# Performance work log

Hardware: AMD Instinct MI355X
Metric: run time of the kernel (lower is better)

## Reference

```python
import jax, jax.numpy as jnp
import numpy as np
import math

D_MODEL = 1024
HEADS = 16
HEAD_DIM = D_MODEL // HEADS
BATCH = 2
SEQ = 2048


def setup_inputs() -> dict:
    key = jax.random.key(0)
    ks = jax.random.split(key, 6)
    scale = 1.0 / math.sqrt(D_MODEL)
    return {
        "x": jax.random.normal(ks[0], (BATCH, SEQ, D_MODEL), dtype=jnp.float32),
        "mask": jnp.zeros((SEQ, SEQ), dtype=jnp.float32),
        "w_qkv": jax.random.normal(ks[1], (D_MODEL, 3 * D_MODEL), dtype=jnp.float32) * scale,
        "b_qkv": jax.random.normal(ks[2], (3 * D_MODEL,), dtype=jnp.float32) * 0.01,
        "w_out": jax.random.normal(ks[3], (D_MODEL, D_MODEL), dtype=jnp.float32) * scale,
        "b_out": jax.random.normal(ks[4], (D_MODEL,), dtype=jnp.float32) * 0.01,
    }


def reference(x, mask, w_qkv, b_qkv, w_out, b_out):
    B, S, D = x.shape
    H, hd = HEADS, HEAD_DIM
    # fused QKV projection: [B,S,3D]
    qkv = x @ w_qkv + b_qkv
    # [B,S,H,3*hd] -> [B,H,S,3*hd]
    qkv = qkv.reshape(B, S, H, 3 * hd).transpose(0, 2, 1, 3)
    q, k, v = jnp.split(qkv, 3, axis=-1)  # each [B,H,S,hd]
    inv_sqrt_d = jnp.asarray(1.0 / math.sqrt(hd), dtype=x.dtype)
    scores = jnp.einsum("bhqd,bhkd->bhqk", q, k) * inv_sqrt_d
    # additive mask; [S,S] broadcasts identically in [H,B,S,S] or [B,H,S,S] layout
    scores = scores + mask
    attn = jax.nn.softmax(scores, axis=-1)
    vals = jnp.einsum("bhqk,bhkd->bhqd", attn, v)  # [B,H,S,hd]
    vals = vals.transpose(0, 2, 1, 3).reshape(B, S, H * hd)
    return vals @ w_out + b_out
```

## Files before the change

kernel.cpp:

```cpp
#include <hip/hip_runtime.h>


typedef __bf16 bf16;
typedef __bf16 bf16x2 __attribute__((ext_vector_type(2)));
typedef __bf16 bf16x4 __attribute__((ext_vector_type(4)));
typedef __bf16 bf16x8 __attribute__((ext_vector_type(8)));
typedef float f32x4 __attribute__((ext_vector_type(4)));
typedef float f32x16 __attribute__((ext_vector_type(16)));

#define MFMA(a, b, c) __builtin_amdgcn_mfma_f32_16x16x32_bf16((a), (b), (c), 0, 0, 0)
#define MFMA32(a, b, c) __builtin_amdgcn_mfma_f32_32x32x16_bf16((a), (b), (c), 0, 0, 0)

#if __has_builtin(__builtin_amdgcn_exp2f)
#define EXP2(x) __builtin_amdgcn_exp2f(x)
#else
#define EXP2(x) exp2f(x)
#endif

__device__ __forceinline__ void load_lds16(const bf16* g, void* l) {
    __builtin_amdgcn_global_load_lds(
        (const __attribute__((address_space(1))) unsigned int*)g,
        (__attribute__((address_space(3))) unsigned int*)l, 16, 0, 0);
}

__global__ void cast4_kernel(const float* __restrict__ in, bf16* __restrict__ out, int n4) {
    int i = blockIdx.x * blockDim.x + threadIdx.x;
    if (i < n4) {
        float4 v = ((const float4*)in)[i];
        bf16x4 o = {(bf16)v.x, (bf16)v.y, (bf16)v.z, (bf16)v.w};
        ((bf16x4*)out)[i] = o;
    }
}

__global__ void transpose_cast_kernel(const float* __restrict__ in, bf16* __restrict__ out,
                                      int R, int C) {
    __shared__ float tile[32][33];
    int bx = blockIdx.x * 32;
    int by = blockIdx.y * 32;
    int tx = threadIdx.x, ty = threadIdx.y;
    for (int i = 0; i < 32; i += 8)
        tile[ty + i][tx] = in[(size_t)(by + ty + i) * C + bx + tx];
    __syncthreads();
    for (int i = 0; i < 32; i += 8)
        out[(size_t)(bx + ty + i) * R + by + tx] = (bf16)tile[tx][ty + i];
}

__global__ __launch_bounds__(256) void gemm_qkv_kernel(
    const bf16* __restrict__ A, const bf16* __restrict__ BT,
    const float* __restrict__ bias,
    bf16* __restrict__ Q, bf16* __restrict__ K, bf16* __restrict__ VT) {
    __shared__ __attribute__((aligned(16))) char lds[2][16384];
    int bm = blockIdx.x, bn = blockIdx.y;
    int t = threadIdx.x;
    int w = t >> 6, lane = t & 63, g = lane >> 4, l16 = lane & 15;
    int wm = (w >> 1) * 64, wn = (w & 1) * 64;
    f32x4 acc[4][4] = {};
    const bf16* Ablk = A + (size_t)(bm * 128) * 1024;
    const bf16* Bblk = BT + (size_t)(bn * 128) * 1024;
    int srow = t >> 2;
    int scg = (t & 3) ^ (srow & 3);
    const bf16* ag0 = Ablk + (size_t)srow * 1024 + scg * 8;
    const bf16* ag1 = ag0 + 64 * 1024;
    const bf16* bg0 = Bblk + (size_t)srow * 1024 + scg * 8;
    const bf16* bg1 = bg0 + 64 * 1024;

    load_lds16(ag0, lds[0] + t * 16);
    load_lds16(ag1, lds[0] + 4096 + t * 16);
    load_lds16(bg0, lds[0] + 8192 + t * 16);
    load_lds16(bg1, lds[0] + 12288 + t * 16);
    asm volatile("s_waitcnt vmcnt(0)" ::: "memory");

    int sw = l16 & 3;
#pragma unroll 2
    for (int j = 0; j < 32; j++) {
        asm volatile("s_barrier" ::: "memory");
        int jp = j + 1 < 32 ? j + 1 : 31;
        char* dst = lds[(j + 1) & 1];
        load_lds16(ag0 + jp * 32, dst + t * 16);
        load_lds16(ag1 + jp * 32, dst + 4096 + t * 16);
        load_lds16(bg0 + jp * 32, dst + 8192 + t * 16);
        load_lds16(bg1 + jp * 32, dst + 12288 + t * 16);

        const bf16* As = (const bf16*)lds[j & 1];
        const bf16* Bs = (const bf16*)(lds[j & 1] + 8192);
        bf16x8 af[4], bfr[4];
#pragma unroll
        for (int mi = 0; mi < 4; mi++) {
            int row = wm + mi * 16 + l16;
            af[mi] = *(const bf16x8*)(&As[row * 32 + (g ^ sw) * 8]);
        }
#pragma unroll
        for (int ni = 0; ni < 4; ni++) {
            int row = wn + ni * 16 + l16;
            bfr[ni] = *(const bf16x8*)(&Bs[row * 32 + (g ^ sw) * 8]);
        }
#pragma unroll
        for (int mi = 0; mi < 4; mi++)
#pragma unroll
            for (int ni = 0; ni < 4; ni++)
                acc[mi][ni] = MFMA(bfr[ni], af[mi], acc[mi][ni]);
        asm volatile("s_waitcnt vmcnt(0)" ::: "memory");
    }
    __syncthreads();

    bf16* vt = (bf16*)lds;
    int b = bm >> 4;
    int row0 = (bm & 15) * 128 + wm;
    int half_col = bn * 128 + wn;
    int h = half_col / 192, tt = half_col % 192;
    size_t bh = (size_t)(b * 16 + h);

    if (tt < 128) {
        bf16* base = (tt == 0 ? Q : K) + bh * 2048 * 64;
#pragma unroll
        for (int mi = 0; mi < 4; mi++) {
#pragma unroll
            for (int ni = 0; ni < 4; ni++) {
                int d0 = ni * 16 + g * 4;
                float4 bv = *(const float4*)(&bias[half_col + d0]);
                int s = row0 + mi * 16 + l16;
                bf16x4 pk = {(bf16)(acc[mi][ni][0] + bv.x), (bf16)(acc[mi][ni][1] + bv.y),
                             (bf16)(acc[mi][ni][2] + bv.z), (bf16)(acc[mi][ni][3] + bv.w)};
                *(bf16x4*)(&base[(size_t)s * 64 + d0]) = pk;
            }
        }
    } else {
#pragma unroll
        for (int mi = 0; mi < 4; mi++) {
            int s_local = wm + mi * 16 + l16;
#pragma unroll
            for (int ni = 0; ni < 4; ni++) {
                int d0 = ni * 16 + g * 4;
                float4 bv = *(const float4*)(&bias[half_col + d0]);
                vt[(d0 + 0) * 136 + s_local] = (bf16)(acc[mi][ni][0] + bv.x);
                vt[(d0 + 1) * 136 + s_local] = (bf16)(acc[mi][ni][1] + bv.y);
                vt[(d0 + 2) * 136 + s_local] = (bf16)(acc[mi][ni][2] + bv.z);
                vt[(d0 + 3) * 136 + s_local] = (bf16)(acc[mi][ni][3] + bv.w);
            }
        }
    }
    __syncthreads();

    int hc0 = bn * 128, hc1 = bn * 128 + 64;
    int vhalf = (hc0 % 192 == 128) ? 0 : ((hc1 % 192 == 128) ? 1 : -1);
    if (vhalf >= 0) {
        int vcol = bn * 128 + vhalf * 64;
        size_t vbh = (size_t)(b * 16 + vcol / 192);
        int d = t >> 2, ch = t & 3;
        const bf16* src = &vt[d * 136 + ch * 32];
        bf16* dstp = &VT[(vbh * 64 + d) * 2048 + (bm & 15) * 128 + ch * 32];
#pragma unroll
        for (int k = 0; k < 4; k++)
            *(bf16x8*)(&dstp[k * 8]) = *(const bf16x8*)(&src[k * 8]);
    }
}

__global__ __launch_bounds__(256) void gemm_out_kernel(
    const bf16* __restrict__ A, const bf16* __restrict__ BT,
    const float* __restrict__ bias, float* __restrict__ out) {
    __shared__ __attribute__((aligned(16))) char lds[2][12288];
    int bm = blockIdx.x, bn = blockIdx.y;
    int t = threadIdx.x;
    int w = t >> 6, lane = t & 63, g = lane >> 4, l16 = lane & 15;
    int wm = (w >> 1) * 64, wn = (w & 1) * 32;
    f32x4 acc[4][2] = {};
    const bf16* Ablk = A + (size_t)(bm * 128) * 1024;
    const bf16* Bblk = BT + (size_t)(bn * 64) * 1024;
    int srow = t >> 2;
    int scg = (t & 3) ^ (srow & 3);
    const bf16* ag0 = Ablk + (size_t)srow * 1024 + scg * 8;
    const bf16* ag1 = ag0 + 64 * 1024;
    const bf16* bg0 = Bblk + (size_t)srow * 1024 + scg * 8;

    load_lds16(ag0, lds[0] + t * 16);
    load_lds16(ag1, lds[0] + 4096 + t * 16);
    load_lds16(bg0, lds[0] + 8192 + t * 16);
    asm volatile("s_waitcnt vmcnt(0)" ::: "memory");

    int sw = l16 & 3;
#pragma unroll 2
    for (int j = 0; j < 32; j++) {
        asm volatile("s_barrier" ::: "memory");
        int jp = j + 1 < 32 ? j + 1 : 31;
        char* dst = lds[(j + 1) & 1];
        load_lds16(ag0 + jp * 32, dst + t * 16);
        load_lds16(ag1 + jp * 32, dst + 4096 + t * 16);
        load_lds16(bg0 + jp * 32, dst + 8192 + t * 16);

        const bf16* As = (const bf16*)lds[j & 1];
        const bf16* Bs = (const bf16*)(lds[j & 1] + 8192);
        bf16x8 af[4], bfr[2];
#pragma unroll
        for (int mi = 0; mi < 4; mi++) {
            int row = wm + mi * 16 + l16;
            af[mi] = *(const bf16x8*)(&As[row * 32 + (g ^ sw) * 8]);
        }
#pragma unroll
        for (int ni = 0; ni < 2; ni++) {
            int row = wn + ni * 16 + l16;
            bfr[ni] = *(const bf16x8*)(&Bs[row * 32 + (g ^ sw) * 8]);
        }
#pragma unroll
        for (int mi = 0; mi < 4; mi++)
#pragma unroll
            for (int ni = 0; ni < 2; ni++)
                acc[mi][ni] = MFMA(bfr[ni], af[mi], acc[mi][ni]);
        asm volatile("s_waitcnt vmcnt(0)" ::: "memory");
    }

#pragma unroll
    for (int mi = 0; mi < 4; mi++) {
#pragma unroll
        for (int ni = 0; ni < 2; ni++) {
            int row = bm * 128 + wm + mi * 16 + l16;
            int col0 = bn * 64 + wn + ni * 16 + g * 4;
            float4 bv = *(const float4*)(&bias[col0]);
            float4 ov = {acc[mi][ni][0] + bv.x, acc[mi][ni][1] + bv.y,
                         acc[mi][ni][2] + bv.z, acc[mi][ni][3] + bv.w};
            *(float4*)(&out[(size_t)row * 1024 + col0]) = ov;
        }
    }
}

__global__ __launch_bounds__(256, 2) void attn_kernel(
    const bf16* __restrict__ Q, const bf16* __restrict__ K,
    const bf16* __restrict__ VT, const float* __restrict__ mask,
    bf16* __restrict__ vals) {
    __shared__ __attribute__((aligned(16))) char lds[4][8192];

    int blk = blockIdx.x;
    int bh = ((blk & 7) << 2) | ((blk >> 3) & 3);
    int qt = blk >> 5;
    int t = threadIdx.x;
    int w = t >> 6, lane = t & 63;
    int l32 = lane & 31, hi = lane >> 5;
    int qw = qt * 128 + w * 32;

    const bf16* Qp = Q + (size_t)bh * 2048 * 64;
    const bf16* Kp = K + (size_t)bh * 2048 * 64;
    const bf16* Vp = VT + (size_t)bh * 64 * 2048;
    const float* mrow = mask + (size_t)(qw + l32) * 2048;

    int ks_row = t >> 3;
    int ks_cblk = (t & 7) ^ (ks_row & 7);
    const bf16* kg = Kp + ks_row * 64 + ks_cblk * 8;
    int vs_d = t >> 2;
    int vs_sblk = (t & 3) ^ ((t >> 3) & 3);
    const bf16* vg = Vp + (size_t)vs_d * 2048 + vs_sblk * 8;

    const float SCL = 0.125f * 1.44269504089f;
    const float L2E = 1.44269504089f;

    bf16x8 qf[4];
#pragma unroll
    for (int t4 = 0; t4 < 4; t4++)
        qf[t4] = *(const bf16x8*)(&Qp[(size_t)(qw + l32) * 64 + t4 * 16 + hi * 8]);

    load_lds16(kg + 0, lds[0] + t * 16);
    load_lds16(vg + 0, lds[0] + 4096 + t * 16);
    float4 mc0 = *(const float4*)(&mrow[0 + hi * 4]);
    float4 mc1 = *(const float4*)(&mrow[8 + hi * 4]);
    float4 mc2 = *(const float4*)(&mrow[16 + hi * 4]);
    float4 mc3 = *(const float4*)(&mrow[24 + hi * 4]);
    load_lds16(kg + 32 * 64, lds[1] + t * 16);
    load_lds16(vg + 32, lds[1] + 4096 + t * 16);
    asm volatile("s_waitcnt vmcnt(0)" ::: "memory");
    asm volatile("s_barrier" ::: "memory");

    f32x16 o0 = {}, o1 = {};
    const f32x16 kZero = {};
    float la = 0.f;

    for (int j = 0; j < 64; j++) {
        const char* bufp = lds[j & 3];
        int jm = j + 1 < 64 ? j + 1 : 63;
        float4 nm0 = *(const float4*)(&mrow[jm * 32 + 0 + hi * 4]);
        float4 nm1 = *(const float4*)(&mrow[jm * 32 + 8 + hi * 4]);
        float4 nm2 = *(const float4*)(&mrow[jm * 32 + 16 + hi * 4]);
        float4 nm3 = *(const float4*)(&mrow[jm * 32 + 24 + hi * 4]);
        int jp = j + 2 < 64 ? j + 2 : 63;
        char* dstp = lds[(j + 2) & 3];
        load_lds16(kg + (size_t)jp * 32 * 64, dstp + t * 16);
        load_lds16(vg + jp * 32, dstp + 4096 + t * 16);
        asm volatile("s_waitcnt vmcnt(12)" ::: "memory");
        asm volatile("s_barrier" ::: "memory");

        f32x16 s;
        {
            int slot0 = l32 * 8 + ((2 * 0 + hi) ^ (l32 & 7));
            bf16x8 kf0 = *(const bf16x8*)(&bufp[slot0 * 16]);
            s = MFMA32(kf0, qf[0], kZero);
            int slot1 = l32 * 8 + ((2 * 1 + hi) ^ (l32 & 7));
            bf16x8 kf1 = *(const bf16x8*)(&bufp[slot1 * 16]);
            s = MFMA32(kf1, qf[1], s);
            int slot2 = l32 * 8 + ((2 * 2 + hi) ^ (l32 & 7));
            bf16x8 kf2 = *(const bf16x8*)(&bufp[slot2 * 16]);
            s = MFMA32(kf2, qf[2], s);
            int slot3 = l32 * 8 + ((2 * 3 + hi) ^ (l32 & 7));
            bf16x8 kf3 = *(const bf16x8*)(&bufp[slot3 * 16]);
            s = MFMA32(kf3, qf[3], s);
        }

        float p[16];
        p[0]  = EXP2(s[0] * SCL + mc0.x * L2E);
        p[1]  = EXP2(s[1] * SCL + mc0.y * L2E);
        p[2]  = EXP2(s[2] * SCL + mc0.z * L2E);
        p[3]  = EXP2(s[3] * SCL + mc0.w * L2E);
        p[4]  = EXP2(s[4] * SCL + mc1.x * L2E);
        p[5]  = EXP2(s[5] * SCL + mc1.y * L2E);
        p[6]  = EXP2(s[6] * SCL + mc1.z * L2E);
        p[7]  = EXP2(s[7] * SCL + mc1.w * L2E);
        p[8]  = EXP2(s[8] * SCL + mc2.x * L2E);
        p[9]  = EXP2(s[9] * SCL + mc2.y * L2E);
        p[10] = EXP2(s[10] * SCL + mc2.z * L2E);
        p[11] = EXP2(s[11] * SCL + mc2.w * L2E);
        p[12] = EXP2(s[12] * SCL + mc3.x * L2E);
        p[13] = EXP2(s[13] * SCL + mc3.y * L2E);
        p[14] = EXP2(s[14] * SCL + mc3.z * L2E);
        p[15] = EXP2(s[15] * SCL + mc3.w * L2E);
        {
            float a0 = p[0] + p[1], a1 = p[2] + p[3], a2 = p[4] + p[5], a3 = p[6] + p[7];
            float a4 = p[8] + p[9], a5 = p[10] + p[11], a6 = p[12] + p[13], a7 = p[14] + p[15];
            float b0 = a0 + a1, b1 = a2 + a3, b2 = a4 + a5, b3 = a6 + a7;
            la += (b0 + b1) + (b2 + b3);
        }

        unsigned dw0, dw1, dw2, dw3, dw4, dw5, dw6, dw7;
        {
            union { bf16x2 h; unsigned u; } u;
            u.h = bf16x2{(bf16)p[0],  (bf16)p[1]};  dw0 = u.u;
            u.h = bf16x2{(bf16)p[2],  (bf16)p[3]};  dw1 = u.u;
            u.h = bf16x2{(bf16)p[4],  (bf16)p[5]};  dw2 = u.u;
            u.h = bf16x2{(bf16)p[6],  (bf16)p[7]};  dw3 = u.u;
            u.h = bf16x2{(bf16)p[8],  (bf16)p[9]};  dw4 = u.u;
            u.h = bf16x2{(bf16)p[10], (bf16)p[11]}; dw5 = u.u;
            u.h = bf16x2{(bf16)p[12], (bf16)p[13]}; dw6 = u.u;
            u.h = bf16x2{(bf16)p[14], (bf16)p[15]}; dw7 = u.u;
        }
        int sx0 = __shfl_xor((int)dw0, 32, 64);
        int sx1 = __shfl_xor((int)dw1, 32, 64);
        int sx2 = __shfl_xor((int)dw2, 32, 64);
        int sx3 = __shfl_xor((int)dw3, 32, 64);
        int sx4 = __shfl_xor((int)dw4, 32, 64);
        int sx5 = __shfl_xor((int)dw5, 32, 64);
        int sx6 = __shfl_xor((int)dw6, 32, 64);
        int sx7 = __shfl_xor((int)dw7, 32, 64);
        bool hib = hi != 0;
        union { unsigned u[4]; bf16x8 v; } pb0, pb1;
        pb0.u[0] = hib ? (unsigned)sx2 : dw0;
        pb0.u[1] = hib ? (unsigned)sx3 : dw1;
        pb0.u[2] = hib ? dw2 : (unsigned)sx0;
        pb0.u[3] = hib ? dw3 : (unsigned)sx1;
        pb1.u[0] = hib ? (unsigned)sx6 : dw4;
        pb1.u[1] = hib ? (unsigned)sx7 : dw5;
        pb1.u[2] = hib ? dw6 : (unsigned)sx4;
        pb1.u[3] = hib ? dw7 : (unsigned)sx5;

        {
            int d0 = l32;
            int d1 = 32 + l32;
            int sv00 = d0 * 4 + ((2 * 0 + hi) ^ ((d0 >> 1) & 3));
            int sv01 = d0 * 4 + ((2 * 1 + hi) ^ ((d0 >> 1) & 3));
            int sv10 = d1 * 4 + ((2 * 0 + hi) ^ ((d1 >> 1) & 3));
            int sv11 = d1 * 4 + ((2 * 1 + hi) ^ ((d1 >> 1) & 3));
            bf16x8 vf00 = *(const bf16x8*)(&bufp[4096 + sv00 * 16]);
            bf16x8 vf01 = *(const bf16x8*)(&bufp[4096 + sv01 * 16]);
            bf16x8 vf10 = *(const bf16x8*)(&bufp[4096 + sv10 * 16]);
            bf16x8 vf11 = *(const bf16x8*)(&bufp[4096 + sv11 * 16]);
            o0 = MFMA32(vf00, pb0.v, o0);
            o0 = MFMA32(vf01, pb1.v, o0);
            o1 = MFMA32(vf10, pb0.v, o1);
            o1 = MFMA32(vf11, pb1.v, o1);
        }

        mc0 = nm0; mc1 = nm1; mc2 = nm2; mc3 = nm3;
    }
    asm volatile("s_waitcnt vmcnt(0)" ::: "memory");

    la += __shfl_xor(la, 32, 64);
    int b = bh >> 4, hh = bh & 15;
    float li = 1.f / la;
    size_t row = (size_t)(b * 2048 + qw + l32);
#pragma unroll
    for (int rg = 0; rg < 4; rg++) {
        bf16x4 pk0 = {(bf16)(o0[rg * 4 + 0] * li), (bf16)(o0[rg * 4 + 1] * li),
                      (bf16)(o0[rg * 4 + 2] * li), (bf16)(o0[rg * 4 + 3] * li)};
        *(bf16x4*)(&vals[row * 1024 + hh * 64 + rg * 8 + hi * 4]) = pk0;
        bf16x4 pk1 = {(bf16)(o1[rg * 4 + 0] * li), (bf16)(o1[rg * 4 + 1] * li),
                      (bf16)(o1[rg * 4 + 2] * li), (bf16)(o1[rg * 4 + 3] * li)};
        *(bf16x4*)(&vals[row * 1024 + hh * 64 + 32 + rg * 8 + hi * 4]) = pk1;
    }
}

extern "C" void kernel_launch(void* const* d_in, const int* in_sizes, int n_in,
                              void* d_out, int out_size, void* d_ws, size_t ws_size,
                              hipStream_t stream) {
    const float* x     = (const float*)d_in[0];
    const float* mask  = (const float*)d_in[1];
    const float* w_qkv = (const float*)d_in[2];
    const float* b_qkv = (const float*)d_in[3];
    const float* w_out = (const float*)d_in[4];
    const float* b_out = (const float*)d_in[5];
    float* out = (float*)d_out;

    char* ws = (char*)d_ws;
    size_t off = 0;
    bf16* xb    = (bf16*)(ws + off); off += (size_t)4096 * 1024 * 2;
    bf16* wqkvT = (bf16*)(ws + off); off += (size_t)3072 * 1024 * 2;
    bf16* woutT = (bf16*)(ws + off); off += (size_t)1024 * 1024 * 2;
    bf16* Qa    = (bf16*)(ws + off); off += (size_t)32 * 2048 * 64 * 2;
    bf16* Ka    = (bf16*)(ws + off); off += (size_t)32 * 2048 * 64 * 2;
    bf16* VTa   = (bf16*)(ws + off); off += (size_t)32 * 64 * 2048 * 2;
    bf16* vals  = (bf16*)(ws + off); off += (size_t)4096 * 1024 * 2;

    cast4_kernel<<<4096, 256, 0, stream>>>(x, xb, 4096 * 1024 / 4);
    transpose_cast_kernel<<<dim3(96, 32), dim3(32, 8), 0, stream>>>(w_qkv, wqkvT, 1024, 3072);
    transpose_cast_kernel<<<dim3(32, 32), dim3(32, 8), 0, stream>>>(w_out, woutT, 1024, 1024);
    gemm_qkv_kernel<<<dim3(32, 24), 256, 0, stream>>>(xb, wqkvT, b_qkv, Qa, Ka, VTa);
    attn_kernel<<<512, 256, 0, stream>>>(Qa, Ka, VTa, mask, vals);
    gemm_out_kernel<<<dim3(32, 16), 256, 0, stream>>>(vals, woutT, b_out, out);
}
```

Measured before the change: 225.3 us.

## Software-pipeline PV MFMA one iteration behind QK in attention loop

Defers the P·V MFMAs of iteration j into iteration j+1, issuing them alongside the next QK^T MFMAs so the matrix unit can overlap with exp/softmax work. V fragments are loaded into registers at the end of each iteration, and a final PV step is added after the loop. It also halves the cross-lane shuffles by selecting which dword to exchange before the shuffle, and hoists the swizzled LDS offsets out of the loop. Carrying P and V fragments across iterations raises register pressure, which could lower occupancy. The buffer ring must not overwrite a V tile before it has been read.

```diff
diff --git a/kernel.cpp b/kernel.cpp
--- a/kernel.cpp
+++ b/kernel.cpp
@@ -271,6 +271,22 @@
     const f32x16 kZero = {};
     float la = 0.f;
 
+    union { unsigned u[4]; bf16x8 v; } pp0, pp1;
+    pp0.u[0] = 0; pp0.u[1] = 0; pp0.u[2] = 0; pp0.u[3] = 0;
+    pp1.u[0] = 0; pp1.u[1] = 0; pp1.u[2] = 0; pp1.u[3] = 0;
+    bf16x8 vfp0 = {}, vfp1 = {}, vfp2 = {}, vfp3 = {};
+
+    int slot0 = (l32 * 8 + ((2 * 0 + hi) ^ (l32 & 7))) * 16;
+    int slot1 = (l32 * 8 + ((2 * 1 + hi) ^ (l32 & 7))) * 16;
+    int slot2 = (l32 * 8 + ((2 * 2 + hi) ^ (l32 & 7))) * 16;
+    int slot3 = (l32 * 8 + ((2 * 3 + hi) ^ (l32 & 7))) * 16;
+    int d0l = l32, d1l = 32 + l32;
+    int sv00 = 4096 + (d0l * 4 + ((2 * 0 + hi) ^ ((d0l >> 1) & 3))) * 16;
+    int sv01 = 4096 + (d0l * 4 + ((2 * 1 + hi) ^ ((d0l >> 1) & 3))) * 16;
+    int sv10 = 4096 + (d1l * 4 + ((2 * 0 + hi) ^ ((d1l >> 1) & 3))) * 16;
+    int sv11 = 4096 + (d1l * 4 + ((2 * 1 + hi) ^ ((d1l >> 1) & 3))) * 16;
+    bool hib = hi != 0;
+
     for (int j = 0; j < 64; j++) {
         const char* bufp = lds[j & 3];
         int jm = j + 1 < 64 ? j + 1 : 63;
@@ -285,21 +301,21 @@
         asm volatile("s_waitcnt vmcnt(12)" ::: "memory");
         asm volatile("s_barrier" ::: "memory");
 
+        bf16x8 kf0 = *(const bf16x8*)(&bufp[slot0]);
+        bf16x8 kf1 = *(const bf16x8*)(&bufp[slot1]);
+        bf16x8 kf2 = *(const bf16x8*)(&bufp[slot2]);
+        bf16x8 kf3 = *(const bf16x8*)(&bufp[slot3]);
+
+        o0 = MFMA32(vfp0, pp0.v, o0);
+        o0 = MFMA32(vfp1, pp1.v, o0);
+        o1 = MFMA32(vfp2, pp0.v, o1);
+        o1 = MFMA32(vfp3, pp1.v, o1);
+
         f32x16 s;
-        {
-            int slot0 = l32 * 8 + ((2 * 0 + hi) ^ (l32 & 7));
-            bf16x8 kf0 = *(const bf16x8*)(&bufp[slot0 * 16]);
-            s = MFMA32(kf0, qf[0], kZero);
-            int slot1 = l32 * 8 + ((2 * 1 + hi) ^ (l32 & 7));
-            bf16x8 kf1 = *(const bf16x8*)(&bufp[slot1 * 16]);
-            s = MFMA32(kf1, qf[1], s);
-            int slot2 = l32 * 8 + ((2 * 2 + hi) ^ (l32 & 7));
-            bf16x8 kf2 = *(const bf16x8*)(&bufp[slot2 * 16]);
-            s = MFMA32(kf2, qf[2], s);
-            int slot3 = l32 * 8 + ((2 * 3 + hi) ^ (l32 & 7));
-            bf16x8 kf3 = *(const bf16x8*)(&bufp[slot3 * 16]);
-            s = MFMA32(kf3, qf[3], s);
-        }
+        s = MFMA32(kf0, qf[0], kZero);
+        s = MFMA32(kf1, qf[1], s);
+        s = MFMA32(kf2, qf[2], s);
+        s = MFMA32(kf3, qf[3], s);
 
         float p[16];
         p[0]  = EXP2(s[0] * SCL + mc0.x * L2E);
@@ -337,44 +353,30 @@
             u.h = bf16x2{(bf16)p[12], (bf16)p[13]}; dw6 = u.u;
             u.h = bf16x2{(bf16)p[14], (bf16)p[15]}; dw7 = u.u;
         }
-        int sx0 = __shfl_xor((int)dw0, 32, 64);
-        int sx1 = __shfl_xor((int)dw1, 32, 64);
-        int sx2 = __shfl_xor((int)dw2, 32, 64);
-        int sx3 = __shfl_xor((int)dw3, 32, 64);
-        int sx4 = __shfl_xor((int)dw4, 32, 64);
-        int sx5 = __shfl_xor((int)dw5, 32, 64);
-        int sx6 = __shfl_xor((int)dw6, 32, 64);
-        int sx7 = __shfl_xor((int)dw7, 32, 64);
-        bool hib = hi != 0;
-        union { unsigned u[4]; bf16x8 v; } pb0, pb1;
-        pb0.u[0] = hib ? (unsigned)sx2 : dw0;
-        pb0.u[1] = hib ? (unsigned)sx3 : dw1;
-        pb0.u[2] = hib ? dw2 : (unsigned)sx0;
-        pb0.u[3] = hib ? dw3 : (unsigned)sx1;
-        pb1.u[0] = hib ? (unsigned)sx6 : dw4;
-        pb1.u[1] = hib ? (unsigned)sx7 : dw5;
-        pb1.u[2] = hib ? dw6 : (unsigned)sx4;
-        pb1.u[3] = hib ? dw7 : (unsigned)sx5;
-
-        {
-            int d0 = l32;
-            int d1 = 32 + l32;
-            int sv00 = d0 * 4 + ((2 * 0 + hi) ^ ((d0 >> 1) & 3));
-            int sv01 = d0 * 4 + ((2 * 1 + hi) ^ ((d0 >> 1) & 3));
-            int sv10 = d1 * 4 + ((2 * 0 + hi) ^ ((d1 >> 1) & 3));
-            int sv11 = d1 * 4 + ((2 * 1 + hi) ^ ((d1 >> 1) & 3));
-            bf16x8 vf00 = *(const bf16x8*)(&bufp[4096 + sv00 * 16]);
-            bf16x8 vf01 = *(const bf16x8*)(&bufp[4096 + sv01 * 16]);
-            bf16x8 vf10 = *(const bf16x8*)(&bufp[4096 + sv10 * 16]);
-            bf16x8 vf11 = *(const bf16x8*)(&bufp[4096 + sv11 * 16]);
-            o0 = MFMA32(vf00, pb0.v, o0);
-            o0 = MFMA32(vf01, pb1.v, o0);
-            o1 = MFMA32(vf10, pb0.v, o1);
-            o1 = MFMA32(vf11, pb1.v, o1);
-        }
+        unsigned r0 = (unsigned)__shfl_xor((int)(hib ? dw0 : dw2), 32, 64);
+        unsigned r1 = (unsigned)__shfl_xor((int)(hib ? dw1 : dw3), 32, 64);
+        unsigned r2 = (unsigned)__shfl_xor((int)(hib ? dw4 : dw6), 32, 64);
+        unsigned r3 = (unsigned)__shfl_xor((int)(hib ? dw5 : dw7), 32, 64);
+        pp0.u[0] = hib ? r0 : dw0;
+        pp0.u[1] = hib ? r1 : dw1;
+        pp0.u[2] = hib ? dw2 : r0;
+        pp0.u[3] = hib ? dw3 : r1;
+        pp1.u[0] = hib ? r2 : dw4;
+        pp1.u[1] = hib ? r3 : dw5;
+        pp1.u[2] = hib ? dw6 : r2;
+        pp1.u[3] = hib ? dw7 : r3;
+
+        vfp0 = *(const bf16x8*)(&bufp[sv00]);
+        vfp1 = *(const bf16x8*)(&bufp[sv01]);
+        vfp2 = *(const bf16x8*)(&bufp[sv10]);
+        vfp3 = *(const bf16x8*)(&bufp[sv11]);
 
         mc0 = nm0; mc1 = nm1; mc2 = nm2; mc3 = nm3;
     }
+    o0 = MFMA32(vfp0, pp0.v, o0);
+    o0 = MFMA32(vfp1, pp1.v, o0);
+    o1 = MFMA32(vfp2, pp0.v, o1);
+    o1 = MFMA32(vfp3, pp1.v, o1);
     asm volatile("s_waitcnt vmcnt(0)" ::: "memory");
 
     la += __shfl_xor(la, 32, 64);
```

Result: slower. 231.9 us (+2.9%).
